# Kernel tuning notes

Measured on AMD Instinct MI355X. Metric: run time of the kernel, lower is better.

Reference implementation:

```python
import jax, jax.numpy as jnp
import numpy as np

NEG_WEIGHT = 0.5   # args_config.lambda_
REG_WEIGHT = 1e-4  # args_config.l2 (dropout rate 0.0 -> identity)

N_USERS, N_ITEMS, DIM = 200000, 1000000, 64
BATCH, HIST = 4096, 200


def setup_inputs() -> dict:
    key = jax.random.key(0)
    k1, k2, k3, k4, k5 = jax.random.split(key, 5)
    users = jax.random.randint(k1, (BATCH,), 0, N_USERS, dtype=jnp.int64 if jax.config.jax_enable_x64 else jnp.int32).astype(jnp.int32)
    hist = jax.random.randint(k2, (N_USERS, HIST), 0, N_ITEMS).astype(jnp.int32)
    user_emb = jax.random.normal(k3, (N_USERS, DIM), dtype=jnp.float32) * 0.1
    item_emb = jax.random.normal(k4, (N_ITEMS, DIM), dtype=jnp.float32) * 0.1
    Hw = jax.random.normal(k5, (1, DIM), dtype=jnp.float32) * 0.1
    return {"users": users, "hist": hist, "user_emb": user_emb,
            "item_emb": item_emb, "Hw": Hw}


def reference(users, hist, user_emb, item_emb, Hw):
    h = Hw[0]                                   # [D]
    u = user_emb[users]                         # [B, D]
    items = item_emb[hist[users]]               # [B, L, D]
    # pos_score[b,l] = sum_d u[b,d] * items[b,l,d] * h[d]  (mul + H_i linear)
    pos_score = jnp.einsum('bd,bld,d->bl', u, items, h)
    # Gram matrices replace bmm(outer).sum(0): E^T E, U_b^T U_b, h h^T
    item_sum = item_emb.T @ item_emb            # [D, D]
    user_sum = u.T @ u                          # [D, D]
    H_sum = jnp.outer(h, h)                     # [D, D]
    t = jnp.sum(item_sum * user_sum * H_sum)
    loss = NEG_WEIGHT * t
    loss = loss + jnp.sum((1.0 - NEG_WEIGHT) * jnp.square(pos_score) - 2.0 * pos_score)
    # reg: 2-norm (Frobenius) of each full embedding table
    reg_loss = REG_WEIGHT * (jnp.linalg.norm(user_emb) + jnp.linalg.norm(item_emb))
    loss = loss + reg_loss
    return (loss, reg_loss, reg_loss)
```

## Files before the change

### kernel.cpp

```cpp
#include <hip/hip_runtime.h>
#include <hip/hip_bf16.h>

typedef __bf16 bf16x8 __attribute__((ext_vector_type(8)));
typedef float f32x16 __attribute__((ext_vector_type(16)));

template<bool GATHER>
static __device__ __forceinline__ void gram_body(
    const float* __restrict__ emb, const int* __restrict__ idx,
    int nrows, int nwaves_total, int blk,
    float* __restrict__ partial, float* __restrict__ red, int t) {
    const int lane = t & 63, wave = t >> 6;
    const int c = lane & 31, kh = lane >> 5;
    const int wid = blk * 4 + wave;
    const int step = nwaves_total * 16;

    f32x16 g00 = {}, g01 = {}, g11 = {};
    float cur0[8], cur1[8];

    int k0 = wid * 16;
    if (k0 < nrows) {
        const int kb = k0 + kh * 8;
#pragma unroll
        for (int j = 0; j < 8; ++j) {
            const size_t rb = (GATHER ? (size_t)idx[kb + j] : (size_t)(kb + j)) * 64;
            cur0[j] = emb[rb + c];
            cur1[j] = emb[rb + 32 + c];
        }
    }
    for (; k0 < nrows; k0 += step) {
        float nx0[8], nx1[8];
        const int k1 = k0 + step;
        if (k1 < nrows) {
            const int kb = k1 + kh * 8;
#pragma unroll
            for (int j = 0; j < 8; ++j) {
                const size_t rb = (GATHER ? (size_t)idx[kb + j] : (size_t)(kb + j)) * 64;
                nx0[j] = emb[rb + c];
                nx1[j] = emb[rb + 32 + c];
            }
        } else {
#pragma unroll
            for (int j = 0; j < 8; ++j) { nx0[j] = 0.f; nx1[j] = 0.f; }
        }
        bf16x8 f0, f1;
#pragma unroll
        for (int j = 0; j < 8; ++j) {
            f0[j] = (__bf16)cur0[j];
            f1[j] = (__bf16)cur1[j];
        }
        g00 = __builtin_amdgcn_mfma_f32_32x32x16_bf16(f0, f0, g00, 0, 0, 0);
        g01 = __builtin_amdgcn_mfma_f32_32x32x16_bf16(f0, f1, g01, 0, 0, 0);
        g11 = __builtin_amdgcn_mfma_f32_32x32x16_bf16(f1, f1, g11, 0, 0, 0);
#pragma unroll
        for (int j = 0; j < 8; ++j) { cur0[j] = nx0[j]; cur1[j] = nx1[j]; }
    }

    __syncthreads();
    for (int w = 0; w < 4; ++w) {
        if (wave == w) {
#pragma unroll
            for (int r = 0; r < 16; ++r) {
                const int cell = ((r & 3) + 8 * (r >> 2) + 4 * kh) * 32 + c;
                if (w == 0) {
                    red[cell] = g00[r]; red[1024 + cell] = g01[r]; red[2048 + cell] = g11[r];
                } else {
                    red[cell] += g00[r]; red[1024 + cell] += g01[r]; red[2048 + cell] += g11[r];
                }
            }
        }
        __syncthreads();
    }
    float* outp = partial + (size_t)blk * 3072;
    for (int i = t; i < 3072; i += 256) outp[i] = red[i];
}

__global__ __launch_bounds__(256, 4) void fused_kernel(
    const int* __restrict__ users, const int* __restrict__ hist,
    const float* __restrict__ user_emb, const float* __restrict__ item_emb,
    const float* __restrict__ Hw,
    int n_users, int n_items, int batch, int histL,
    int NA, int NP, int NSS, int NU,
    float* __restrict__ partA, float* __restrict__ partB,
    float* __restrict__ p1, float* __restrict__ p2, float* __restrict__ pss) {
    __shared__ float red[3072];
    const int bid = blockIdx.x, t = threadIdx.x;

    if (bid < NA) {
        gram_body<false>(item_emb, nullptr, n_items, NA * 4, bid,
                         partA, red, t);
    } else if (bid < NA + NP) {
        const int pid = bid - NA;
        const int lane = t & 63, wave = t >> 6;
        const int k = lane & 15, g = lane >> 4;
        for (int w = pid * 4 + wave; w < batch; w += NP * 4) {
            const int iu = users[w];
            const float4 vu = *reinterpret_cast<const float4*>(user_emb + (size_t)iu * 64 + k * 4);
            const float4 vh = *reinterpret_cast<const float4*>(Hw + k * 4);
            const float4 uh = make_float4(vu.x * vh.x, vu.y * vh.y, vu.z * vh.z, vu.w * vh.w);
            const int* hrow = hist + (size_t)iu * histL;

            float s1 = 0.f, s2 = 0.f;
            int l = g;
            for (; l + 12 < histL; l += 16) {
                int it[4];
#pragma unroll
                for (int u = 0; u < 4; ++u) it[u] = hrow[l + 4 * u];
                float d[4];
#pragma unroll
                for (int u = 0; u < 4; ++u) {
                    const float4 v = *reinterpret_cast<const float4*>(
                        item_emb + (size_t)it[u] * 64 + k * 4);
                    d[u] = v.x * uh.x + v.y * uh.y + v.z * uh.z + v.w * uh.w;
                }
#pragma unroll
                for (int u = 0; u < 4; ++u) {
                    float dd = d[u];
                    dd += __shfl_xor(dd, 1, 16);
                    dd += __shfl_xor(dd, 2, 16);
                    dd += __shfl_xor(dd, 4, 16);
                    dd += __shfl_xor(dd, 8, 16);
                    s1 += dd;
                    s2 = fmaf(dd, dd, s2);
                }
            }
            for (; l < histL; l += 4) {
                const int it = hrow[l];
                const float4 v = *reinterpret_cast<const float4*>(
                    item_emb + (size_t)it * 64 + k * 4);
                float dd = v.x * uh.x + v.y * uh.y + v.z * uh.z + v.w * uh.w;
                dd += __shfl_xor(dd, 1, 16);
                dd += __shfl_xor(dd, 2, 16);
                dd += __shfl_xor(dd, 4, 16);
                dd += __shfl_xor(dd, 8, 16);
                s1 += dd;
                s2 = fmaf(dd, dd, s2);
            }
            s1 += __shfl_xor(s1, 16, 64); s1 += __shfl_xor(s1, 32, 64);
            s2 += __shfl_xor(s2, 16, 64); s2 += __shfl_xor(s2, 32, 64);
            if (lane == 0) { p1[w] = s1 * 0.0625f; p2[w] = s2 * 0.0625f; }
        }
    } else if (bid < NA + NP + NSS) {
        const int cid = bid - NA - NP;
        const int n4 = n_users * 16;
        float s = 0.f;
        for (int i = cid * 256 + t; i < n4; i += NSS * 256) {
            const float4 v = reinterpret_cast<const float4*>(user_emb)[i];
            s = fmaf(v.x, v.x, s); s = fmaf(v.y, v.y, s);
            s = fmaf(v.z, v.z, s); s = fmaf(v.w, v.w, s);
        }
#pragma unroll
        for (int off = 32; off >= 1; off >>= 1) s += __shfl_xor(s, off, 64);
        if ((t & 63) == 0) red[t >> 6] = s;
        __syncthreads();
        if (t == 0) pss[cid] = red[0] + red[1] + red[2] + red[3];
    } else {
        gram_body<true>(user_emb, users, batch, NU * 4, bid - NA - NP - NSS,
                        partB, red, t);
    }
}

__global__ __launch_bounds__(256) void reduce_gram_kernel(
    const float* __restrict__ pa, int na,
    const float* __restrict__ pb, int nb, float* __restrict__ part2) {
    const int bid = blockIdx.x;
    const int cellblk = bid % 24, seg = bid / 24;
    const int e = cellblk * 256 + threadIdx.x;
    const float* p; int n, ee;
    if (e < 3072) { p = pa; n = na; ee = e; }
    else          { p = pb; n = nb; ee = e - 3072; }
    const int chunk = (n + 7) >> 3;
    const int b0 = seg * chunk;
    int b1 = b0 + chunk; if (b1 > n) b1 = n;
    float s[4] = {0.f, 0.f, 0.f, 0.f};
    int b = b0;
    for (; b + 4 <= b1; b += 4)
#pragma unroll
        for (int u = 0; u < 4; ++u) s[u] += p[(size_t)(b + u) * 3072 + ee];
    for (; b < b1; ++b) s[0] += p[(size_t)b * 3072 + ee];
    part2[(size_t)seg * 6144 + e] = (s[0] + s[1]) + (s[2] + s[3]);
}

__global__ __launch_bounds__(1024) void finalize_kernel(
    const float* __restrict__ part2, const float* __restrict__ Hw,
    const float* __restrict__ p1, const float* __restrict__ p2, int npos,
    const float* __restrict__ pss, int nss, float* __restrict__ outp) {
    const int t = threadIdx.x;
    float tsum = 0.f, trace = 0.f, s1 = 0.f, s2 = 0.f, su = 0.f;
    for (int e = t; e < 3072; e += 1024) {
        float gi = 0.f, gu = 0.f;
#pragma unroll
        for (int seg = 0; seg < 8; ++seg) {
            gi += part2[(size_t)seg * 6144 + e];
            gu += part2[(size_t)seg * 6144 + 3072 + e];
        }
        const int tile = e >> 10, r = (e & 1023) >> 5, cc = e & 31;
        const int i = (tile == 2) ? r + 32 : r;
        const int j = (tile == 0) ? cc : cc + 32;
        const float w = (tile == 1) ? 2.0f : 1.0f;
        tsum += w * gi * gu * Hw[i] * Hw[j];
        if (i == j) trace += gi;
    }
    for (int e = t; e < npos; e += 1024) { s1 += p1[e]; s2 += p2[e]; }
    for (int e = t; e < nss; e += 1024) su += pss[e];
#pragma unroll
    for (int off = 32; off >= 1; off >>= 1) {
        tsum += __shfl_xor(tsum, off, 64);
        trace += __shfl_xor(trace, off, 64);
        s1 += __shfl_xor(s1, off, 64);
        s2 += __shfl_xor(s2, off, 64);
        su += __shfl_xor(su, off, 64);
    }
    __shared__ float rr[16][5];
    if ((t & 63) == 0) {
        const int w = t >> 6;
        rr[w][0] = tsum; rr[w][1] = trace; rr[w][2] = s1;
        rr[w][3] = s2;   rr[w][4] = su;
    }
    __syncthreads();
    if (t == 0) {
        float a[5] = {0.f, 0.f, 0.f, 0.f, 0.f};
        for (int w = 0; w < 16; ++w)
#pragma unroll
            for (int q = 0; q < 5; ++q) a[q] += rr[w][q];
        const float reg = 1e-4f * (sqrtf(a[4]) + sqrtf(a[1]));
        const float loss = 0.5f * a[0] + 0.5f * a[3] - 2.0f * a[2] + reg;
        outp[0] = loss; outp[1] = reg; outp[2] = reg;
    }
}

extern "C" void kernel_launch(void* const* d_in, const int* in_sizes, int n_in,
                              void* d_out, int out_size, void* d_ws, size_t ws_size,
                              hipStream_t stream) {
    const int*   users    = (const int*)d_in[0];
    const int*   hist     = (const int*)d_in[1];
    const float* user_emb = (const float*)d_in[2];
    const float* item_emb = (const float*)d_in[3];
    const float* Hw       = (const float*)d_in[4];
    float* outp = (float*)d_out;
    float* ws   = (float*)d_ws;

    const int n_users = in_sizes[2] / 64;
    const int n_items = in_sizes[3] / 64;
    const int batch   = in_sizes[0];
    const int histL   = in_sizes[1] / n_users;

    int NA = 512;
    const int NP  = 384;
    const int NSS = 96;
    const int NU  = 32;

    const size_t o_p1 = 0;
    const size_t o_p2 = o_p1 + (size_t)batch;
    const size_t o_ss = o_p2 + (size_t)batch;
    const size_t o_part2 = o_ss + NSS;
    const size_t o_part = o_part2 + 8 * 6144;
    long availf = (long)(ws_size / 4) - (long)o_part - (long)NU * 3072;
    if ((long)NA * 3072 > availf) {
        NA = (int)(availf / 3072);
        if (NA < 8) NA = 8;
    }
    float* partA = ws + o_part;
    float* partB = partA + (size_t)NA * 3072;

    fused_kernel<<<NA + NP + NSS + NU, 256, 0, stream>>>(
        users, hist, user_emb, item_emb, Hw,
        n_users, n_items, batch, histL,
        NA, NP, NSS, NU,
        partA, partB, ws + o_p1, ws + o_p2, ws + o_ss);
    reduce_gram_kernel<<<24 * 8, 256, 0, stream>>>(
        partA, NA, partB, NU, ws + o_part2);
    finalize_kernel<<<1, 1024, 0, stream>>>(
        ws + o_part2, Hw, ws + o_p1, ws + o_p2, batch,
        ws + o_ss, NSS, outp);
}
```

Measured before the change: 110.0 us.

## Fuse gram reduction and finalize into one kernel with last-block atomics

Replaces the two-stage reduce_gram and single-block finalize kernels with one 12-block kernel. Each thread sums all partial Gram tiles for one cell, then accumulates the scalars via atomics, and the last block to finish computes the loss. This removes a kernel launch and the intermediate part2 buffer, but adds a memset and cuts reduction parallelism from 192 blocks to 12.

```diff
diff --git a/kernel.cpp b/kernel.cpp
--- a/kernel.cpp
+++ b/kernel.cpp
@@ -159,49 +159,38 @@
     }
 }
 
-__global__ __launch_bounds__(256) void reduce_gram_kernel(
+__global__ __launch_bounds__(256) void reduce_finalize_kernel(
     const float* __restrict__ pa, int na,
-    const float* __restrict__ pb, int nb, float* __restrict__ part2) {
-    const int bid = blockIdx.x;
-    const int cellblk = bid % 24, seg = bid / 24;
-    const int e = cellblk * 256 + threadIdx.x;
-    const float* p; int n, ee;
-    if (e < 3072) { p = pa; n = na; ee = e; }
-    else          { p = pb; n = nb; ee = e - 3072; }
-    const int chunk = (n + 7) >> 3;
-    const int b0 = seg * chunk;
-    int b1 = b0 + chunk; if (b1 > n) b1 = n;
-    float s[4] = {0.f, 0.f, 0.f, 0.f};
-    int b = b0;
-    for (; b + 4 <= b1; b += 4)
-#pragma unroll
-        for (int u = 0; u < 4; ++u) s[u] += p[(size_t)(b + u) * 3072 + ee];
-    for (; b < b1; ++b) s[0] += p[(size_t)b * 3072 + ee];
-    part2[(size_t)seg * 6144 + e] = (s[0] + s[1]) + (s[2] + s[3]);
-}
-
-__global__ __launch_bounds__(1024) void finalize_kernel(
-    const float* __restrict__ part2, const float* __restrict__ Hw,
+    const float* __restrict__ pb, int nb,
+    const float* __restrict__ Hw,
     const float* __restrict__ p1, const float* __restrict__ p2, int npos,
-    const float* __restrict__ pss, int nss, float* __restrict__ outp) {
-    const int t = threadIdx.x;
-    float tsum = 0.f, trace = 0.f, s1 = 0.f, s2 = 0.f, su = 0.f;
-    for (int e = t; e < 3072; e += 1024) {
-        float gi = 0.f, gu = 0.f;
-#pragma unroll
-        for (int seg = 0; seg < 8; ++seg) {
-            gi += part2[(size_t)seg * 6144 + e];
-            gu += part2[(size_t)seg * 6144 + 3072 + e];
-        }
-        const int tile = e >> 10, r = (e & 1023) >> 5, cc = e & 31;
-        const int i = (tile == 2) ? r + 32 : r;
-        const int j = (tile == 0) ? cc : cc + 32;
-        const float w = (tile == 1) ? 2.0f : 1.0f;
-        tsum += w * gi * gu * Hw[i] * Hw[j];
-        if (i == j) trace += gi;
-    }
-    for (int e = t; e < npos; e += 1024) { s1 += p1[e]; s2 += p2[e]; }
-    for (int e = t; e < nss; e += 1024) su += pss[e];
+    const float* __restrict__ pss, int nss,
+    float* __restrict__ acc, float* __restrict__ outp) {
+    const int bid = blockIdx.x, t = threadIdx.x;
+    const int e = bid * 256 + t;
+
+    float gi4[4] = {0.f, 0.f, 0.f, 0.f};
+    int b = 0;
+    for (; b + 4 <= na; b += 4)
+#pragma unroll
+        for (int u = 0; u < 4; ++u) gi4[u] += pa[(size_t)(b + u) * 3072 + e];
+    for (; b < na; ++b) gi4[0] += pa[(size_t)b * 3072 + e];
+    const float gi = (gi4[0] + gi4[1]) + (gi4[2] + gi4[3]);
+    float gu = 0.f;
+    for (b = 0; b < nb; ++b) gu += pb[(size_t)b * 3072 + e];
+
+    const int tile = e >> 10, r = (e & 1023) >> 5, cc = e & 31;
+    const int i = (tile == 2) ? r + 32 : r;
+    const int j = (tile == 0) ? cc : cc + 32;
+    const float w = (tile == 1) ? 2.0f : 1.0f;
+    float tsum = w * gi * gu * Hw[i] * Hw[j];
+    float trace = (i == j) ? gi : 0.f;
+
+    float s1 = 0.f, s2 = 0.f, su = 0.f;
+    if (bid == 0) {
+        for (int q = t; q < npos; q += 256) { s1 += p1[q]; s2 += p2[q]; }
+        for (int q = t; q < nss; q += 256) su += pss[q];
+    }
 #pragma unroll
     for (int off = 32; off >= 1; off >>= 1) {
         tsum += __shfl_xor(tsum, off, 64);
@@ -210,20 +199,36 @@
         s2 += __shfl_xor(s2, off, 64);
         su += __shfl_xor(su, off, 64);
     }
-    __shared__ float rr[16][5];
+    __shared__ float rr[4][5];
     if ((t & 63) == 0) {
-        const int w = t >> 6;
-        rr[w][0] = tsum; rr[w][1] = trace; rr[w][2] = s1;
-        rr[w][3] = s2;   rr[w][4] = su;
+        const int wv = t >> 6;
+        rr[wv][0] = tsum; rr[wv][1] = trace; rr[wv][2] = s1;
+        rr[wv][3] = s2;   rr[wv][4] = su;
     }
     __syncthreads();
+    __shared__ int last;
     if (t == 0) {
-        float a[5] = {0.f, 0.f, 0.f, 0.f, 0.f};
-        for (int w = 0; w < 16; ++w)
-#pragma unroll
-            for (int q = 0; q < 5; ++q) a[q] += rr[w][q];
-        const float reg = 1e-4f * (sqrtf(a[4]) + sqrtf(a[1]));
-        const float loss = 0.5f * a[0] + 0.5f * a[3] - 2.0f * a[2] + reg;
+        atomicAdd(&acc[1], rr[0][0] + rr[1][0] + rr[2][0] + rr[3][0]);
+        atomicAdd(&acc[2], rr[0][1] + rr[1][1] + rr[2][1] + rr[3][1]);
+        if (bid == 0) {
+            atomicAdd(&acc[3], rr[0][2] + rr[1][2] + rr[2][2] + rr[3][2]);
+            atomicAdd(&acc[4], rr[0][3] + rr[1][3] + rr[2][3] + rr[3][3]);
+            atomicAdd(&acc[5], rr[0][4] + rr[1][4] + rr[2][4] + rr[3][4]);
+        }
+        __threadfence();
+        const unsigned old = atomicAdd((unsigned*)&acc[0], 1u);
+        last = (old == (unsigned)(gridDim.x - 1)) ? 1 : 0;
+    }
+    __syncthreads();
+    if (last && t == 0) {
+        __threadfence();
+        const float a_t  = atomicAdd(&acc[1], 0.f);
+        const float a_tr = atomicAdd(&acc[2], 0.f);
+        const float a_s1 = atomicAdd(&acc[3], 0.f);
+        const float a_s2 = atomicAdd(&acc[4], 0.f);
+        const float a_su = atomicAdd(&acc[5], 0.f);
+        const float reg = 1e-4f * (sqrtf(a_su) + sqrtf(a_tr));
+        const float loss = 0.5f * a_t + 0.5f * a_s2 - 2.0f * a_s1 + reg;
         outp[0] = loss; outp[1] = reg; outp[2] = reg;
     }
 }
@@ -249,11 +254,11 @@
     const int NSS = 96;
     const int NU  = 32;
 
-    const size_t o_p1 = 0;
+    const size_t o_acc = 0;
+    const size_t o_p1 = 8;
     const size_t o_p2 = o_p1 + (size_t)batch;
     const size_t o_ss = o_p2 + (size_t)batch;
-    const size_t o_part2 = o_ss + NSS;
-    const size_t o_part = o_part2 + 8 * 6144;
+    const size_t o_part = o_ss + NSS;
     long availf = (long)(ws_size / 4) - (long)o_part - (long)NU * 3072;
     if ((long)NA * 3072 > availf) {
         NA = (int)(availf / 3072);
@@ -262,14 +267,14 @@
     float* partA = ws + o_part;
     float* partB = partA + (size_t)NA * 3072;
 
+    hipMemsetAsync(ws + o_acc, 0, 32, stream);
     fused_kernel<<<NA + NP + NSS + NU, 256, 0, stream>>>(
         users, hist, user_emb, item_emb, Hw,
         n_users, n_items, batch, histL,
         NA, NP, NSS, NU,
         partA, partB, ws + o_p1, ws + o_p2, ws + o_ss);
-    reduce_gram_kernel<<<24 * 8, 256, 0, stream>>>(
-        partA, NA, partB, NU, ws + o_part2);
-    finalize_kernel<<<1, 1024, 0, stream>>>(
-        ws + o_part2, Hw, ws + o_p1, ws + o_p2, batch,
-        ws + o_ss, NSS, outp);
-}
+    reduce_finalize_kernel<<<12, 256, 0, stream>>>(
+        partA, NA, partB, NU, Hw,
+        ws + o_p1, ws + o_p2, batch, ws + o_ss, NSS,
+        ws + o_acc, outp);
+}
```

Result: slower. 162.4 us (+47.7%).

## Invert item gather into CSR so pos-score reuses streamed item rows

Applied to the files above, without the earlier changes.

Replaces the per-user random gather of 819K item rows with an inverted index. Six new pre-pass kernels (histogram with atomics, scan, scatter) build a CSR list mapping each item to the batch rows that reference it. The item Gram pass, which already streams the whole item table, then computes the dot products for each listed user against the item row it has loaded. The goal is to remove the random item-table gather traffic, at the cost of several extra launches, atomic-heavy histogram and scatter passes over 819K pairs, divergent inner loops, and serialized shuffle reductions inside the Gram loop.

```diff
diff --git a/kernel.cpp b/kernel.cpp
--- a/kernel.cpp
+++ b/kernel.cpp
@@ -4,11 +4,115 @@
 typedef __bf16 bf16x8 __attribute__((ext_vector_type(8)));
 typedef float f32x16 __attribute__((ext_vector_type(16)));
 
-template<bool GATHER>
+
+__global__ __launch_bounds__(256) void prep_kernel(
+    const int* __restrict__ users, const float* __restrict__ user_emb,
+    const float* __restrict__ Hw, int batch, unsigned npad,
+    float* __restrict__ Up, unsigned* __restrict__ counts) {
+    const int bid = blockIdx.x, t = threadIdx.x;
+    if (bid < 64) {
+        const int n = batch * 64;
+        for (int e = bid * 256 + t; e < n; e += 64 * 256) {
+            const int b = e >> 6, d = e & 63;
+            Up[e] = user_emb[(size_t)users[b] * 64 + d] * Hw[d];
+        }
+    } else {
+        const unsigned nb = gridDim.x - 64;
+        for (unsigned i = (bid - 64) * 256 + t; i <= npad; i += nb * 256)
+            counts[i] = 0u;
+    }
+}
+
+__global__ __launch_bounds__(256) void hist_kernel(
+    const int* __restrict__ users, const int* __restrict__ hist,
+    int batch, int histL, unsigned* __restrict__ counts) {
+    const int n = batch * histL;
+    const int stride = gridDim.x * 256;
+    for (int e = blockIdx.x * 256 + threadIdx.x; e < n; e += stride) {
+        const int b = e / histL, l = e - b * histL;
+        const int it = hist[(size_t)users[b] * histL + l];
+        atomicAdd(&counts[it], 1u);
+    }
+}
+
+__global__ __launch_bounds__(256) void bsum_kernel(
+    const unsigned* __restrict__ counts, unsigned* __restrict__ btot) {
+    const int t = threadIdx.x;
+    const unsigned base = blockIdx.x * 1024;
+    unsigned s = 0;
+    for (int i = t; i < 1024; i += 256) s += counts[base + i];
+#pragma unroll
+    for (int off = 32; off >= 1; off >>= 1) s += __shfl_xor(s, off, 64);
+    __shared__ unsigned r[4];
+    if ((t & 63) == 0) r[t >> 6] = s;
+    __syncthreads();
+    if (t == 0) btot[blockIdx.x] = r[0] + r[1] + r[2] + r[3];
+}
+
+__global__ __launch_bounds__(1024) void scan_kernel(
+    const unsigned* __restrict__ btot, int nblk, unsigned* __restrict__ boff) {
+    const int t = threadIdx.x;
+    __shared__ unsigned sh[1024];
+    const unsigned v = (t < nblk) ? btot[t] : 0u;
+    sh[t] = v;
+    __syncthreads();
+    for (int off = 1; off < 1024; off <<= 1) {
+        const unsigned a = (t >= off) ? sh[t - off] : 0u;
+        __syncthreads();
+        sh[t] += a;
+        __syncthreads();
+    }
+    if (t < nblk) boff[t] = sh[t] - v;
+    if (t == nblk - 1) boff[nblk] = sh[t];
+}
+
+__global__ __launch_bounds__(256) void off_kernel(
+    const unsigned* __restrict__ counts, const unsigned* __restrict__ boff,
+    unsigned npad, unsigned* __restrict__ offsets, unsigned* __restrict__ cursor) {
+    const int bid = blockIdx.x, t = threadIdx.x;
+    const unsigned i0 = bid * 1024 + t * 4;
+    const unsigned c0 = counts[i0], c1 = counts[i0 + 1],
+                   c2 = counts[i0 + 2], c3 = counts[i0 + 3];
+    const unsigned tot = c0 + c1 + c2 + c3;
+    __shared__ unsigned sh[256];
+    sh[t] = tot;
+    __syncthreads();
+    for (int off = 1; off < 256; off <<= 1) {
+        const unsigned a = (t >= off) ? sh[t - off] : 0u;
+        __syncthreads();
+        sh[t] += a;
+        __syncthreads();
+    }
+    const unsigned o = boff[bid] + sh[t] - tot;
+    offsets[i0] = o;                 cursor[i0] = o;
+    offsets[i0 + 1] = o + c0;        cursor[i0 + 1] = o + c0;
+    offsets[i0 + 2] = o + c0 + c1;   cursor[i0 + 2] = o + c0 + c1;
+    offsets[i0 + 3] = o + c0 + c1 + c2; cursor[i0 + 3] = o + c0 + c1 + c2;
+    if (i0 + 4 == npad) offsets[npad] = boff[gridDim.x];
+}
+
+__global__ __launch_bounds__(256) void scatter_kernel(
+    const int* __restrict__ users, const int* __restrict__ hist,
+    int batch, int histL, unsigned* __restrict__ cursor,
+    unsigned* __restrict__ vals) {
+    const int n = batch * histL;
+    const int stride = gridDim.x * 256;
+    for (int e = blockIdx.x * 256 + threadIdx.x; e < n; e += stride) {
+        const int b = e / histL, l = e - b * histL;
+        const int it = hist[(size_t)users[b] * histL + l];
+        const unsigned p = atomicAdd(&cursor[it], 1u);
+        vals[p] = (unsigned)b;
+    }
+}
+
+template<bool GATHER, bool DOPOS>
 static __device__ __forceinline__ void gram_body(
     const float* __restrict__ emb, const int* __restrict__ idx,
     int nrows, int nwaves_total, int blk,
-    float* __restrict__ partial, float* __restrict__ red, int t) {
+    const unsigned* __restrict__ offsets, const unsigned* __restrict__ vals,
+    const float* __restrict__ Up,
+    float* __restrict__ partial, float* __restrict__ ps1, float* __restrict__ ps2,
+    float* __restrict__ red, float* __restrict__ rs, int t) {
     const int lane = t & 63, wave = t >> 6;
     const int c = lane & 31, kh = lane >> 5;
     const int wid = blk * 4 + wave;
@@ -16,6 +120,7 @@
 
     f32x16 g00 = {}, g01 = {}, g11 = {};
     float cur0[8], cur1[8];
+    float s1 = 0.f, s2 = 0.f;
 
     int k0 = wid * 16;
     if (k0 < nrows) {
@@ -51,8 +156,33 @@
         g00 = __builtin_amdgcn_mfma_f32_32x32x16_bf16(f0, f0, g00, 0, 0, 0);
         g01 = __builtin_amdgcn_mfma_f32_32x32x16_bf16(f0, f1, g01, 0, 0, 0);
         g11 = __builtin_amdgcn_mfma_f32_32x32x16_bf16(f1, f1, g11, 0, 0, 0);
+        if (DOPOS) {
+            const int rbase = k0 + kh * 8;
+#pragma unroll
+            for (int j = 0; j < 8; ++j) {
+                const unsigned o0 = offsets[rbase + j];
+                const unsigned o1 = offsets[rbase + j + 1];
+                for (unsigned e = o0; e < o1; ++e) {
+                    const int b = (int)vals[e];
+                    float dd = fmaf(cur0[j], Up[b * 64 + c],
+                                    cur1[j] * Up[b * 64 + 32 + c]);
+                    dd += __shfl_xor(dd, 1, 32);
+                    dd += __shfl_xor(dd, 2, 32);
+                    dd += __shfl_xor(dd, 4, 32);
+                    dd += __shfl_xor(dd, 8, 32);
+                    dd += __shfl_xor(dd, 16, 32);
+                    s1 += dd;
+                    s2 = fmaf(dd, dd, s2);
+                }
+            }
+        }
 #pragma unroll
         for (int j = 0; j < 8; ++j) { cur0[j] = nx0[j]; cur1[j] = nx1[j]; }
+    }
+
+    if (DOPOS) {
+        s1 += __shfl_xor(s1, 32, 64);
+        s2 += __shfl_xor(s2, 32, 64);
     }
 
     __syncthreads();
@@ -67,80 +197,36 @@
                     red[cell] += g00[r]; red[1024 + cell] += g01[r]; red[2048 + cell] += g11[r];
                 }
             }
+            if (DOPOS && lane == 0) {
+                if (w == 0) { rs[0] = s1; rs[1] = s2; }
+                else        { rs[0] += s1; rs[1] += s2; }
+            }
         }
         __syncthreads();
     }
     float* outp = partial + (size_t)blk * 3072;
     for (int i = t; i < 3072; i += 256) outp[i] = red[i];
+    if (DOPOS && t == 0) { ps1[blk] = rs[0]; ps2[blk] = rs[1]; }
 }
 
 __global__ __launch_bounds__(256, 4) void fused_kernel(
-    const int* __restrict__ users, const int* __restrict__ hist,
-    const float* __restrict__ user_emb, const float* __restrict__ item_emb,
-    const float* __restrict__ Hw,
-    int n_users, int n_items, int batch, int histL,
-    int NA, int NP, int NSS, int NU,
+    const int* __restrict__ users, const float* __restrict__ user_emb,
+    const float* __restrict__ item_emb,
+    int n_users, int n_items, int batch,
+    int NA, int NSS, int NU,
+    const unsigned* __restrict__ offsets, const unsigned* __restrict__ vals,
+    const float* __restrict__ Up,
     float* __restrict__ partA, float* __restrict__ partB,
-    float* __restrict__ p1, float* __restrict__ p2, float* __restrict__ pss) {
+    float* __restrict__ ps1, float* __restrict__ ps2, float* __restrict__ pss) {
     __shared__ float red[3072];
+    __shared__ float rs[2];
     const int bid = blockIdx.x, t = threadIdx.x;
 
     if (bid < NA) {
-        gram_body<false>(item_emb, nullptr, n_items, NA * 4, bid,
-                         partA, red, t);
-    } else if (bid < NA + NP) {
-        const int pid = bid - NA;
-        const int lane = t & 63, wave = t >> 6;
-        const int k = lane & 15, g = lane >> 4;
-        for (int w = pid * 4 + wave; w < batch; w += NP * 4) {
-            const int iu = users[w];
-            const float4 vu = *reinterpret_cast<const float4*>(user_emb + (size_t)iu * 64 + k * 4);
-            const float4 vh = *reinterpret_cast<const float4*>(Hw + k * 4);
-            const float4 uh = make_float4(vu.x * vh.x, vu.y * vh.y, vu.z * vh.z, vu.w * vh.w);
-            const int* hrow = hist + (size_t)iu * histL;
-
-            float s1 = 0.f, s2 = 0.f;
-            int l = g;
-            for (; l + 12 < histL; l += 16) {
-                int it[4];
-#pragma unroll
-                for (int u = 0; u < 4; ++u) it[u] = hrow[l + 4 * u];
-                float d[4];
-#pragma unroll
-                for (int u = 0; u < 4; ++u) {
-                    const float4 v = *reinterpret_cast<const float4*>(
-                        item_emb + (size_t)it[u] * 64 + k * 4);
-                    d[u] = v.x * uh.x + v.y * uh.y + v.z * uh.z + v.w * uh.w;
-                }
-#pragma unroll
-                for (int u = 0; u < 4; ++u) {
-                    float dd = d[u];
-                    dd += __shfl_xor(dd, 1, 16);
-                    dd += __shfl_xor(dd, 2, 16);
-                    dd += __shfl_xor(dd, 4, 16);
-                    dd += __shfl_xor(dd, 8, 16);
-                    s1 += dd;
-                    s2 = fmaf(dd, dd, s2);
-                }
-            }
-            for (; l < histL; l += 4) {
-                const int it = hrow[l];
-                const float4 v = *reinterpret_cast<const float4*>(
-                    item_emb + (size_t)it * 64 + k * 4);
-                float dd = v.x * uh.x + v.y * uh.y + v.z * uh.z + v.w * uh.w;
-                dd += __shfl_xor(dd, 1, 16);
-                dd += __shfl_xor(dd, 2, 16);
-                dd += __shfl_xor(dd, 4, 16);
-                dd += __shfl_xor(dd, 8, 16);
-                s1 += dd;
-                s2 = fmaf(dd, dd, s2);
-            }
-            s1 += __shfl_xor(s1, 16, 64); s1 += __shfl_xor(s1, 32, 64);
-            s2 += __shfl_xor(s2, 16, 64); s2 += __shfl_xor(s2, 32, 64);
-            if (lane == 0) { p1[w] = s1 * 0.0625f; p2[w] = s2 * 0.0625f; }
-        }
-    } else if (bid < NA + NP + NSS) {
-        const int cid = bid - NA - NP;
+        gram_body<false, true>(item_emb, nullptr, n_items, NA * 4, bid,
+                               offsets, vals, Up, partA, ps1, ps2, red, rs, t);
+    } else if (bid < NA + NSS) {
+        const int cid = bid - NA;
         const int n4 = n_users * 16;
         float s = 0.f;
         for (int i = cid * 256 + t; i < n4; i += NSS * 256) {
@@ -154,8 +240,9 @@
         __syncthreads();
         if (t == 0) pss[cid] = red[0] + red[1] + red[2] + red[3];
     } else {
-        gram_body<true>(user_emb, users, batch, NU * 4, bid - NA - NP - NSS,
-                        partB, red, t);
+        gram_body<true, false>(user_emb, users, batch, NU * 4, bid - NA - NSS,
+                               nullptr, nullptr, nullptr, partB,
+                               nullptr, nullptr, red, rs, t);
     }
 }
 
@@ -244,32 +331,60 @@
     const int batch   = in_sizes[0];
     const int histL   = in_sizes[1] / n_users;
 
-    int NA = 512;
-    const int NP  = 384;
+    const unsigned npad = (unsigned)(((n_items + 1023) >> 10) << 10);
+    const int nblk = (int)(npad >> 10);
+    const int npairs = batch * histL;
+
+    int NA = 896;
     const int NSS = 96;
     const int NU  = 32;
 
-    const size_t o_p1 = 0;
-    const size_t o_p2 = o_p1 + (size_t)batch;
-    const size_t o_ss = o_p2 + (size_t)batch;
-    const size_t o_part2 = o_ss + NSS;
-    const size_t o_part = o_part2 + 8 * 6144;
-    long availf = (long)(ws_size / 4) - (long)o_part - (long)NU * 3072;
+    size_t o = 0;
+    auto alloc = [&](size_t n) { size_t r = o; o += (n + 15) & ~15ull; return r; };
+    const size_t o_up     = alloc((size_t)batch * 64);
+    const size_t o_counts = alloc(npad + 1);
+    const size_t o_off    = alloc(npad + 1);
+    const size_t o_cur    = alloc(npad + 1);
+    const size_t o_btot   = alloc(nblk + 1);
+    const size_t o_boff   = alloc(nblk + 2);
+    const size_t o_vals   = alloc(npairs);
+    const size_t o_ps1    = alloc(NA);
+    const size_t o_ps2    = alloc(NA);
+    const size_t o_pss    = alloc(NSS);
+    const size_t o_part2  = alloc(8 * 6144);
+    const size_t o_partB  = alloc((size_t)NU * 3072);
+    const size_t o_partA  = o;
+    long availf = (long)(ws_size / 4) - (long)o_partA;
     if ((long)NA * 3072 > availf) {
         NA = (int)(availf / 3072);
         if (NA < 8) NA = 8;
     }
-    float* partA = ws + o_part;
-    float* partB = partA + (size_t)NA * 3072;
-
-    fused_kernel<<<NA + NP + NSS + NU, 256, 0, stream>>>(
-        users, hist, user_emb, item_emb, Hw,
-        n_users, n_items, batch, histL,
-        NA, NP, NSS, NU,
-        partA, partB, ws + o_p1, ws + o_p2, ws + o_ss);
+
+    float*    Up      = ws + o_up;
+    unsigned* counts  = (unsigned*)(ws + o_counts);
+    unsigned* offsets = (unsigned*)(ws + o_off);
+    unsigned* cursor  = (unsigned*)(ws + o_cur);
+    unsigned* btot    = (unsigned*)(ws + o_btot);
+    unsigned* boff    = (unsigned*)(ws + o_boff);
+    unsigned* vals    = (unsigned*)(ws + o_vals);
+    float*    partA   = ws + o_partA;
+    float*    partB   = ws + o_partB;
+
+    prep_kernel<<<1024, 256, 0, stream>>>(users, user_emb, Hw, batch, npad,
+                                          Up, counts);
+    hist_kernel<<<400, 256, 0, stream>>>(users, hist, batch, histL, counts);
+    bsum_kernel<<<nblk, 256, 0, stream>>>(counts, btot);
+    scan_kernel<<<1, 1024, 0, stream>>>(btot, nblk, boff);
+    off_kernel<<<nblk, 256, 0, stream>>>(counts, boff, npad, offsets, cursor);
+    scatter_kernel<<<400, 256, 0, stream>>>(users, hist, batch, histL,
+                                            cursor, vals);
+    fused_kernel<<<NA + NSS + NU, 256, 0, stream>>>(
+        users, user_emb, item_emb, n_users, n_items, batch,
+        NA, NSS, NU, offsets, vals, Up,
+        partA, partB, ws + o_ps1, ws + o_ps2, ws + o_pss);
     reduce_gram_kernel<<<24 * 8, 256, 0, stream>>>(
         partA, NA, partB, NU, ws + o_part2);
     finalize_kernel<<<1, 1024, 0, stream>>>(
-        ws + o_part2, Hw, ws + o_p1, ws + o_p2, batch,
-        ws + o_ss, NSS, outp);
-}
+        ws + o_part2, Hw, ws + o_ps1, ws + o_ps2, NA,
+        ws + o_pss, NSS, outp);
+}
```

Result: slower. 305.9 us (+178.1%).
